# Kernel optimization log

Measured on AMD Instinct MI355X. Metric: run time of the kernel, lower is better.

Reference implementation:

```python
import jax, jax.numpy as jnp
import numpy as np

EMB = 128
HEADS = 8
B = 8
T = 2048


def setup_inputs() -> dict:
    key = jax.random.key(0)
    ks = jax.random.split(key, 6)
    x = jax.random.normal(ks[0], (B, T, EMB), dtype=jnp.float32)
    # torch Linear(emb, heads*emb, bias=False): store as (in, out) so y = x @ W
    scale = 1.0 / np.sqrt(EMB)
    Wq = jax.random.uniform(ks[1], (EMB, HEADS * EMB), jnp.float32, -scale, scale)
    Wk = jax.random.uniform(ks[2], (EMB, HEADS * EMB), jnp.float32, -scale, scale)
    Wv = jax.random.uniform(ks[3], (EMB, HEADS * EMB), jnp.float32, -scale, scale)
    so = 1.0 / np.sqrt(HEADS * EMB)
    Wo = jax.random.uniform(ks[4], (HEADS * EMB, EMB), jnp.float32, -so, so)
    bo = jax.random.uniform(ks[5], (EMB,), jnp.float32, -so, so)
    return {"x": x, "Wq": Wq, "Wk": Wk, "Wv": Wv, "Wo": Wo, "bo": bo}


def reference(x, Wq, Wk, Wv, Wo, bo):
    b, t, e = x.shape
    h = HEADS
    q = (x @ Wq).reshape(b, t, h, e)  # [b,t,h,e]
    k = (x @ Wk).reshape(b, t, h, e)
    v = (x @ Wv).reshape(b, t, h, e)
    # scores: [b,h,q,k], scaled by sqrt(e) (per-head dim == emb here)
    scores = jnp.einsum('bqhe,bkhe->bhqk', q, k) / jnp.sqrt(jnp.asarray(e, x.dtype))
    attn = jax.nn.softmax(scores, axis=-1)
    out = jnp.einsum('bhqk,bkhe->bqhe', attn, v).reshape(b, t, h * e)
    return out @ Wo + bo
```

## Files before the change

### kernel.cpp

```cpp
#include <hip/hip_runtime.h>

using bf16x8 = __attribute__((ext_vector_type(8))) short;
using f32x4  = __attribute__((ext_vector_type(4))) float;
using f32x16 = __attribute__((ext_vector_type(16))) float;

__device__ __forceinline__ ushort f2bf(float f) {
    union { float f; unsigned int u; } c; c.f = f;
    unsigned int u = c.u;
    u = (u + 0x7fffu + ((u >> 16) & 1u)) >> 16;
    return (ushort)u;
}

#if defined(__has_builtin)
#if __has_builtin(__builtin_amdgcn_cvt_pk_bf16_f32)
#define HAS_PK_BF16 1
#endif
#if __has_builtin(__builtin_amdgcn_permlane32_swap)
#define HAS_PL32 1
#endif
#endif
__device__ __forceinline__ unsigned int pkbf(float a, float b) {
#ifdef HAS_PK_BF16
    typedef __bf16 bf2 __attribute__((ext_vector_type(2)));
    union { bf2 v; unsigned int u; } cv;
    cv.v = __builtin_amdgcn_cvt_pk_bf16_f32(a, b);
    return cv.u;
#else
    return (unsigned int)f2bf(a) | ((unsigned int)f2bf(b) << 16);
#endif
}

__device__ __forceinline__ void pl32swap(unsigned &a, unsigned &b) {
#ifdef HAS_PL32
    typedef unsigned uint2v __attribute__((ext_vector_type(2)));
    uint2v r = __builtin_amdgcn_permlane32_swap(a, b, false, false);
    a = r.x; b = r.y;
#else
    asm volatile("v_permlane32_swap_b32 %0, %1" : "+v"(a), "+v"(b));
#endif
}

__device__ __forceinline__ void dma16(const ushort* g, ushort* l) {
    __builtin_amdgcn_global_load_lds(
        (const __attribute__((address_space(1))) unsigned int*)g,
        (__attribute__((address_space(3))) unsigned int*)l, 16, 0, 0);
}

constexpr int BB   = 8;
constexpr int HH   = 8;
constexpr int TT   = 2048;
constexpr int DD   = 128;
#define C2F (0.08838834764831845f * 1.4426950408889634f)

__global__ void prep_kernel(const float* __restrict__ x,
                            const float* __restrict__ Wq, const float* __restrict__ Wk,
                            const float* __restrict__ Wv, const float* __restrict__ Wo,
                            ushort* __restrict__ xb, ushort* __restrict__ WqkvT,
                            ushort* __restrict__ WoT) {
    int t = blockIdx.x * 256 + threadIdx.x;
    if (t < 524288) {
        float4 v = ((const float4*)x)[t];
        ushort4 o;
        o.x = f2bf(v.x); o.y = f2bf(v.y); o.z = f2bf(v.z); o.w = f2bf(v.w);
        ((ushort4*)xb)[t] = o;
    } else if (t < 524288 + 393216) {
        int i = t - 524288;
        int j = i >> 7, kk = i & 127;
        const float* W = (j < 1024) ? Wq : ((j < 2048) ? Wk : Wv);
        int jj = j & 1023;
        WqkvT[j * 128 + kk] = f2bf(W[kk * 1024 + jj]);
    } else {
        int i = t - 917504;
        int e = i >> 10, kk = i & 1023;
        WoT[e * 1024 + kk] = f2bf(Wo[kk * 128 + e]);
    }
}

__global__ __launch_bounds__(256, 2)
void qkv_gemm(const ushort* __restrict__ xb, const ushort* __restrict__ WqkvT,
              ushort* __restrict__ q, ushort* __restrict__ k, ushort* __restrict__ vt) {
    __shared__ ushort Al[128 * 136];
    __shared__ ushort Bl[128 * 136];
    const int tid = threadIdx.x;
    const int n0 = blockIdx.x * 128, m0 = blockIdx.y * 128;

    for (int s = tid; s < 2048; s += 256) {
        int row = s >> 4, oct = s & 15;
        *(uint4*)&Al[row * 136 + oct * 8] = *(const uint4*)&xb[m0 * 128 + s * 8];
        *(uint4*)&Bl[row * 136 + oct * 8] = *(const uint4*)&WqkvT[n0 * 128 + s * 8];
    }
    __syncthreads();

    const int w = tid >> 6, lane = tid & 63, l15 = lane & 15, g = lane >> 4;
    const int wm = (w & 1) * 64, wn = (w >> 1) * 64;
    f32x4 acc[4][4] = {};

#pragma unroll
    for (int ks = 0; ks < 4; ks++) {
        bf16x8 af[4], bfr[4];
#pragma unroll
        for (int mb = 0; mb < 4; mb++)
            af[mb] = *(const bf16x8*)&Al[(wm + mb * 16 + l15) * 136 + ks * 32 + g * 8];
#pragma unroll
        for (int nb = 0; nb < 4; nb++)
            bfr[nb] = *(const bf16x8*)&Bl[(wn + nb * 16 + l15) * 136 + ks * 32 + g * 8];
#pragma unroll
        for (int mb = 0; mb < 4; mb++)
#pragma unroll
            for (int nb = 0; nb < 4; nb++)
                acc[mb][nb] = __builtin_amdgcn_mfma_f32_16x16x32_bf16(af[mb], bfr[nb], acc[mb][nb], 0, 0, 0);
    }

    const int which = n0 >> 10;
    const int b = m0 >> 11;
    const int h = (n0 >> 7) & 7;
    const int bh = b * HH + h;
    if (which == 0) {
#pragma unroll
        for (int mb = 0; mb < 4; mb++)
#pragma unroll
            for (int nb = 0; nb < 4; nb++)
#pragma unroll
                for (int r = 0; r < 4; r++) {
                    int t = (m0 + wm + mb * 16 + g * 4 + r) & 2047;
                    int e = wn + nb * 16 + l15;
                    q[((size_t)bh * TT + t) * DD + e] = f2bf(acc[mb][nb][r] * C2F);
                }
    } else if (which == 1) {
#pragma unroll
        for (int mb = 0; mb < 4; mb++)
#pragma unroll
            for (int nb = 0; nb < 4; nb++)
#pragma unroll
                for (int r = 0; r < 4; r++) {
                    int t = (m0 + wm + mb * 16 + g * 4 + r) & 2047;
                    int e = wn + nb * 16 + l15;
                    int esw = ((((e >> 3) ^ (t & 7)) << 3) | (e & 7));
                    k[((size_t)bh * TT + t) * DD + esw] = f2bf(acc[mb][nb][r]);
                }
    } else {
        __syncthreads();
        ushort* Tl = Al;
#pragma unroll
        for (int mb = 0; mb < 4; mb++)
#pragma unroll
            for (int nb = 0; nb < 4; nb++)
#pragma unroll
                for (int r = 0; r < 4; r++)
                    Tl[(wn + nb * 16 + l15) * 136 + wm + mb * 16 + g * 4 + r] = f2bf(acc[mb][nb][r]);
        __syncthreads();
        const int c0 = (m0 & 2047) >> 5;
        for (int s = tid; s < 2048; s += 256) {
            int e = s >> 4, x = s & 15;
            int cl = x >> 2, pos = x & 3;
            int el = e & 15;
            int vsw = (el ^ (el >> 2)) & 3;
            int tsrc = cl * 32 + ((pos ^ vsw) * 8);
            uint4 val = *(const uint4*)&Tl[e * 136 + tsrc];
            *(uint4*)&vt[(size_t)(((bh * 64 + c0 + cl) * 128) + e) * 32 + pos * 8] = val;
        }
    }
}

__global__ __launch_bounds__(256, 3)
void attn_kernel(const ushort* __restrict__ q, const ushort* __restrict__ k,
                 const ushort* __restrict__ vt, ushort* __restrict__ ao) {
    __shared__ ushort Kl[3][32 * 128];
    __shared__ ushort Vl[3][128 * 32];

    const int idx = blockIdx.x;
    const int h = idx & 7, b = (idx >> 3) & 7, qt128 = idx >> 6;
    const int t0 = qt128 * 128;
    const int bh = b * HH + h;
    const ushort* qg  = q  + (size_t)bh * TT * DD;
    const ushort* kg  = k  + (size_t)bh * TT * DD;
    const ushort* vtg = vt + (size_t)bh * 64 * DD * 32;

    const int tid = threadIdx.x, w = tid >> 6, lane = tid & 63;
    const int l31 = lane & 31, hi = lane >> 5, l15 = lane & 15;
    const int swk = lane & 7;
    const int swv = (l15 ^ (l15 >> 2)) & 3;

    bf16x8 qf[8];
#pragma unroll
    for (int ks = 0; ks < 8; ks++)
        qf[ks] = *(const bf16x8*)&qg[(size_t)(t0 + w * 32 + l31) * DD + ks * 16 + hi * 8];

    const int seg = tid * 8;
#pragma unroll
    for (int pc = 0; pc < 2; pc++)
#pragma unroll
        for (int j = 0; j < 2; j++) {
            dma16(kg  + (size_t)pc * 4096 + seg + j * 2048, &Kl[pc][seg + j * 2048]);
            dma16(vtg + (size_t)pc * 4096 + seg + j * 2048, &Vl[pc][seg + j * 2048]);
        }

    f32x16 o[4] = {};
    float ls = 0.0f;

    int cur = 0, nxt = 2;
    for (int c = 0; c < 64; c++) {
        if (c < 63) asm volatile("s_waitcnt vmcnt(4)" ::: "memory");
        else        asm volatile("s_waitcnt vmcnt(0)" ::: "memory");
        __builtin_amdgcn_s_barrier();
        __builtin_amdgcn_sched_barrier(0);

        if (c < 62) {
            const ushort* kn = kg  + (size_t)(c + 2) * 4096;
            const ushort* vn = vtg + (size_t)(c + 2) * 4096;
#pragma unroll
            for (int j = 0; j < 2; j++) {
                dma16(kn + seg + j * 2048, &Kl[nxt][seg + j * 2048]);
                dma16(vn + seg + j * 2048, &Vl[nxt][seg + j * 2048]);
            }
        }

        f32x16 st = {};
        __builtin_amdgcn_s_setprio(1);
#pragma unroll
        for (int ks = 0; ks < 8; ks++) {
            bf16x8 kf = *(const bf16x8*)&Kl[cur][l31 * 128 + (((ks * 2 + hi) ^ swk) * 8)];
            st = __builtin_amdgcn_mfma_f32_32x32x16_bf16(kf, qf[ks], st, 0, 0, 0);
        }
        __builtin_amdgcn_s_setprio(0);

        float p[16];
#pragma unroll
        for (int r = 0; r < 16; r++) p[r] = __builtin_amdgcn_exp2f(st[r]);
        ls += (((p[0] + p[1]) + (p[2] + p[3])) + ((p[4] + p[5]) + (p[6] + p[7])))
            + (((p[8] + p[9]) + (p[10] + p[11])) + ((p[12] + p[13]) + (p[14] + p[15])));
        unsigned a0 = pkbf(p[0],  p[1]),  a1 = pkbf(p[2],  p[3]);
        unsigned a2 = pkbf(p[4],  p[5]),  a3 = pkbf(p[6],  p[7]);
        unsigned a4 = pkbf(p[8],  p[9]),  a5 = pkbf(p[10], p[11]);
        unsigned a6 = pkbf(p[12], p[13]), a7 = pkbf(p[14], p[15]);
        pl32swap(a0, a2); pl32swap(a1, a3);
        pl32swap(a4, a6); pl32swap(a5, a7);
        union { unsigned u[4]; bf16x8 v; } A, B;
        A.u[0] = a0; A.u[1] = a1; A.u[2] = a2; A.u[3] = a3;
        B.u[0] = a4; B.u[1] = a5; B.u[2] = a6; B.u[3] = a7;
        bf16x8 paA = A.v, paB = B.v;

        __builtin_amdgcn_s_setprio(1);
#pragma unroll
        for (int et = 0; et < 4; et++) {
#pragma unroll
            for (int ks2 = 0; ks2 < 2; ks2++) {
                bf16x8 vb = *(const bf16x8*)&Vl[cur][(et * 32 + l31) * 32 + (((ks2 * 2 + hi) ^ swv) * 8)];
                o[et] = __builtin_amdgcn_mfma_f32_32x32x16_bf16(ks2 ? paB : paA, vb, o[et], 0, 0, 0);
            }
        }
        __builtin_amdgcn_s_setprio(0);

        cur = (cur == 2) ? 0 : cur + 1;
        nxt = (nxt == 2) ? 0 : nxt + 1;
    }

    float tot = ls + __shfl_xor(ls, 32);
    const size_t aobase = (size_t)(b * TT) * 1024 + h * 128;
#pragma unroll
    for (int r = 0; r < 16; r++) {
        int ql = (r & 3) + 8 * (r >> 2) + 4 * hi;
        float inv = 1.0f / __shfl(tot, ql, 64);
        int m = t0 + w * 32 + ql;
#pragma unroll
        for (int et = 0; et < 4; et++)
            ao[aobase + (size_t)m * 1024 + et * 32 + l31] = f2bf(o[et][r] * inv);
    }
}

__global__ __launch_bounds__(256, 2)
void outproj_gemm(const ushort* __restrict__ ao, const ushort* __restrict__ WoT,
                  const float* __restrict__ bo, float* __restrict__ out) {
    __shared__ ushort Al[64 * 72];
    __shared__ ushort Bl[64 * 72];
    const int tid = threadIdx.x;
    const int n0 = blockIdx.x * 64, m0 = blockIdx.y * 64;
    const int w = tid >> 6, lane = tid & 63, l15 = lane & 15, g = lane >> 4;
    const int wm = (w & 1) * 32, wn = (w >> 1) * 32;
    f32x4 acc[2][2] = {};

    for (int kc = 0; kc < 16; kc++) {
        int k0 = kc * 64;
        __syncthreads();
        for (int s = tid; s < 512; s += 256) {
            int row = s >> 3, oct = s & 7;
            *(uint4*)&Al[row * 72 + oct * 8] = *(const uint4*)&ao[(size_t)(m0 + row) * 1024 + k0 + oct * 8];
            *(uint4*)&Bl[row * 72 + oct * 8] = *(const uint4*)&WoT[(n0 + row) * 1024 + k0 + oct * 8];
        }
        __syncthreads();
#pragma unroll
        for (int ks = 0; ks < 2; ks++) {
            bf16x8 af[2], bfr[2];
#pragma unroll
            for (int mb = 0; mb < 2; mb++)
                af[mb] = *(const bf16x8*)&Al[(wm + mb * 16 + l15) * 72 + ks * 32 + g * 8];
#pragma unroll
            for (int nb = 0; nb < 2; nb++)
                bfr[nb] = *(const bf16x8*)&Bl[(wn + nb * 16 + l15) * 72 + ks * 32 + g * 8];
#pragma unroll
            for (int mb = 0; mb < 2; mb++)
#pragma unroll
                for (int nb = 0; nb < 2; nb++)
                    acc[mb][nb] = __builtin_amdgcn_mfma_f32_16x16x32_bf16(af[mb], bfr[nb], acc[mb][nb], 0, 0, 0);
        }
    }

#pragma unroll
    for (int mb = 0; mb < 2; mb++)
#pragma unroll
        for (int nb = 0; nb < 2; nb++) {
            int j = n0 + wn + nb * 16 + l15;
            float bias = bo[j];
#pragma unroll
            for (int r = 0; r < 4; r++) {
                int m = m0 + wm + mb * 16 + g * 4 + r;
                out[(size_t)m * 128 + j] = acc[mb][nb][r] + bias;
            }
        }
}

extern "C" void kernel_launch(void* const* d_in, const int* in_sizes, int n_in,
                              void* d_out, int out_size, void* d_ws, size_t ws_size,
                              hipStream_t stream) {
    const float* x  = (const float*)d_in[0];
    const float* Wq = (const float*)d_in[1];
    const float* Wk = (const float*)d_in[2];
    const float* Wv = (const float*)d_in[3];
    const float* Wo = (const float*)d_in[4];
    const float* bo = (const float*)d_in[5];
    float* out = (float*)d_out;

    char* ws = (char*)d_ws;
    ushort* xb    = (ushort*)(ws);
    ushort* WqkvT = (ushort*)(ws + 4194304);
    ushort* WoT   = (ushort*)(ws + 4980736);
    ushort* qb    = (ushort*)(ws + 5242880);
    ushort* kb    = (ushort*)(ws + 38797312);
    ushort* vtb   = (ushort*)(ws + 72351744);
    ushort* ao    = (ushort*)(ws + 105906176);

    prep_kernel<<<4096, 256, 0, stream>>>(x, Wq, Wk, Wv, Wo, xb, WqkvT, WoT);
    qkv_gemm<<<dim3(24, 128), 256, 0, stream>>>(xb, WqkvT, qb, kb, vtb);
    attn_kernel<<<1024, 256, 0, stream>>>(qb, kb, vtb, ao);
    outproj_gemm<<<dim3(2, 256), 256, 0, stream>>>(ao, WoT, bo, out);
}
```

Before: 283.1 us.

## Preload K/V fragments to registers and split DMA issue around extra barriers

Result: faster. 267.7 us, median of 2 (-5.4%).

```diff
diff --git a/kernel.cpp b/kernel.cpp
--- a/kernel.cpp
+++ b/kernel.cpp
@@ -205,24 +205,26 @@
         __builtin_amdgcn_s_barrier();
         __builtin_amdgcn_sched_barrier(0);
 
+        bf16x8 kf[8];
+#pragma unroll
+        for (int ks = 0; ks < 8; ks++)
+            kf[ks] = *(const bf16x8*)&Kl[cur][l31 * 128 + (((ks * 2 + hi) ^ swk) * 8)];
         if (c < 62) {
-            const ushort* kn = kg  + (size_t)(c + 2) * 4096;
-            const ushort* vn = vtg + (size_t)(c + 2) * 4096;
-#pragma unroll
-            for (int j = 0; j < 2; j++) {
+            const ushort* kn = kg + (size_t)(c + 2) * 4096;
+#pragma unroll
+            for (int j = 0; j < 2; j++)
                 dma16(kn + seg + j * 2048, &Kl[nxt][seg + j * 2048]);
-                dma16(vn + seg + j * 2048, &Vl[nxt][seg + j * 2048]);
-            }
-        }
-
+        }
+        __builtin_amdgcn_s_barrier();
+        asm volatile("s_waitcnt lgkmcnt(0)" ::: "memory");
+        __builtin_amdgcn_sched_barrier(0);
         f32x16 st = {};
         __builtin_amdgcn_s_setprio(1);
 #pragma unroll
-        for (int ks = 0; ks < 8; ks++) {
-            bf16x8 kf = *(const bf16x8*)&Kl[cur][l31 * 128 + (((ks * 2 + hi) ^ swk) * 8)];
-            st = __builtin_amdgcn_mfma_f32_32x32x16_bf16(kf, qf[ks], st, 0, 0, 0);
-        }
+        for (int ks = 0; ks < 8; ks++)
+            st = __builtin_amdgcn_mfma_f32_32x32x16_bf16(kf[ks], qf[ks], st, 0, 0, 0);
         __builtin_amdgcn_s_setprio(0);
+        __builtin_amdgcn_s_barrier();
 
         float p[16];
 #pragma unroll
@@ -240,14 +242,26 @@
         B.u[0] = a4; B.u[1] = a5; B.u[2] = a6; B.u[3] = a7;
         bf16x8 paA = A.v, paB = B.v;
 
+        bf16x8 vb[8];
+#pragma unroll
+        for (int et = 0; et < 4; et++)
+#pragma unroll
+            for (int ks2 = 0; ks2 < 2; ks2++)
+                vb[et * 2 + ks2] = *(const bf16x8*)&Vl[cur][(et * 32 + l31) * 32 + (((ks2 * 2 + hi) ^ swv) * 8)];
+        if (c < 62) {
+            const ushort* vn = vtg + (size_t)(c + 2) * 4096;
+#pragma unroll
+            for (int j = 0; j < 2; j++)
+                dma16(vn + seg + j * 2048, &Vl[nxt][seg + j * 2048]);
+        }
+        __builtin_amdgcn_s_barrier();
+        asm volatile("s_waitcnt lgkmcnt(0)" ::: "memory");
+        __builtin_amdgcn_sched_barrier(0);
         __builtin_amdgcn_s_setprio(1);
 #pragma unroll
         for (int et = 0; et < 4; et++) {
-#pragma unroll
-            for (int ks2 = 0; ks2 < 2; ks2++) {
-                bf16x8 vb = *(const bf16x8*)&Vl[cur][(et * 32 + l31) * 32 + (((ks2 * 2 + hi) ^ swv) * 8)];
-                o[et] = __builtin_amdgcn_mfma_f32_32x32x16_bf16(ks2 ? paB : paA, vb, o[et], 0, 0, 0);
-            }
+            o[et] = __builtin_amdgcn_mfma_f32_32x32x16_bf16(paA, vb[et * 2 + 0], o[et], 0, 0, 0);
+            o[et] = __builtin_amdgcn_mfma_f32_32x32x16_bf16(paB, vb[et * 2 + 1], o[et], 0, 0, 0);
         }
         __builtin_amdgcn_s_setprio(0);
 
```
